# Kernel tuning notes

Hardware: AMD Instinct MI355X
Metric: run time of the kernel (lower is better)

The kernel has to match this reference:

```python
import jax, jax.numpy as jnp
import numpy as np

B, D, E, K = 16384, 1024, 8, 2  # tokens, embed_size, experts, top-k
W_IMPORTANCE = 0.01


def setup_inputs() -> dict:
    key = jax.random.key(0)
    ks = jax.random.split(key, 8)
    s = 1.0 / np.sqrt(D)
    return {
        "x": jax.random.normal(ks[0], (B, D), dtype=jnp.float32),   # fused vision features
        "q": jax.random.normal(ks[1], (B, D), dtype=jnp.float32),   # text features
        # cross-attention (seq_len=1) collapses to V then output projection
        "Wv": jax.random.normal(ks[2], (D, D), dtype=jnp.float32) * s,
        "bv": jnp.zeros((D,), dtype=jnp.float32),
        "Wo": jax.random.normal(ks[3], (D, D), dtype=jnp.float32) * s,
        "bo": jnp.zeros((D,), dtype=jnp.float32),
        # gate linear
        "Wg": jax.random.normal(ks[4], (D, E), dtype=jnp.float32) * s,
        "bg": jnp.zeros((E,), dtype=jnp.float32),
        # experts: Linear -> SiLU -> Linear
        "W1": jax.random.normal(ks[5], (E, D, D), dtype=jnp.float32) * s,
        "b1": jnp.zeros((E, D), dtype=jnp.float32),
        "W2": jax.random.normal(ks[6], (E, D, D), dtype=jnp.float32) * s,
        "b2": jnp.zeros((E, D), dtype=jnp.float32),
    }


def reference(x, q, Wv, bv, Wo, bo, Wg, bg, W1, b1, W2, b2):
    # CrossAttention with q_len = kv_len = 1: softmax over a single key is 1,
    # so attention output = out_proj(V(q)).
    att = (q @ Wv + bv) @ Wo + bo                      # (B, D)
    gate_logits = att @ Wg + bg                        # (B, E)
    gate_prob = jax.nn.softmax(gate_logits, axis=-1)   # eval mode: no noise
    top_w, top_i = jax.lax.top_k(gate_prob, K)         # (B, K)
    top_w = jax.nn.softmax(top_w, axis=-1)             # renormalize over top-k

    y = jnp.zeros_like(x)
    for e in range(E):  # small fixed expert count
        w_e = jnp.sum(jnp.where(top_i == e, top_w, 0.0), axis=-1)  # (B,)
        h = jax.nn.silu(x @ W1[e] + b1[e]) @ W2[e] + b2[e]         # (B, D)
        y = y + w_e[:, None] * h

    importance = gate_prob.sum(axis=0)  # (E,)
    importance_loss = W_IMPORTANCE * (jnp.std(importance, ddof=1) / jnp.mean(importance)) ** 2
    return y, gate_prob, importance_loss
```

## Files before the change

### kernel.cpp

```cpp
#include <hip/hip_runtime.h>
#include <hip/hip_bf16.h>

#define Btok 16384
#define Ddim 1024
#define Eexp 8

typedef __attribute__((ext_vector_type(8))) short short8;
typedef __attribute__((ext_vector_type(4))) float f32x4;

__device__ inline unsigned short f2bf(float f) {
    unsigned int u = __float_as_uint(f);
    unsigned int r = (u + 0x7fffu + ((u >> 16) & 1u)) >> 16;
    return (unsigned short)r;
}

__device__ inline void gload16(const void* g, void* l) {
    __builtin_amdgcn_global_load_lds(
        (const __attribute__((address_space(1))) void*)g,
        (__attribute__((address_space(3))) void*)l, 16, 0, 0);
}

#define MEMF() asm volatile("" ::: "memory")
#define BARRIER() do { MEMF(); __builtin_amdgcn_s_barrier(); MEMF(); } while (0)
#define VMW(n) do { asm volatile("s_waitcnt vmcnt(" #n ")" ::: "memory"); \
                    __builtin_amdgcn_sched_barrier(0); } while (0)

__global__ __launch_bounds__(256) void k_tmp(const float* __restrict__ Wo,
                                             const float* __restrict__ Wg,
                                             float* __restrict__ tmp) {
    int id = blockIdx.x * 256 + threadIdx.x;
    int d = id >> 3, e = id & 7;
    double s = 0.0;
    for (int k = 0; k < Ddim; ++k)
        s += (double)Wo[(long)d * Ddim + k] * (double)Wg[k * Eexp + e];
    tmp[id] = (float)s;
}

__global__ __launch_bounds__(256) void k_wc(const float* __restrict__ Wv,
                                            const float* __restrict__ tmp,
                                            float* __restrict__ WcT) {
    int id = blockIdx.x * 256 + threadIdx.x;
    int d = id >> 3, e = id & 7;
    double s = 0.0;
    for (int k = 0; k < Ddim; ++k)
        s += (double)Wv[(long)d * Ddim + k] * (double)tmp[k * Eexp + e];
    WcT[e * Ddim + d] = (float)s;
}

__global__ __launch_bounds__(512) void k_bc(const float* __restrict__ bv,
                                            const float* __restrict__ bo,
                                            const float* __restrict__ bg,
                                            const float* __restrict__ Wg,
                                            const float* __restrict__ tmp,
                                            float* __restrict__ bcomb) {
    int w = threadIdx.x >> 6, l = threadIdx.x & 63;
    double s = 0.0;
    for (int k = l; k < Ddim; k += 64)
        s += (double)bv[k] * (double)tmp[k * Eexp + w] +
             (double)bo[k] * (double)Wg[k * Eexp + w];
    #pragma unroll
    for (int off = 32; off; off >>= 1) s += __shfl_xor(s, off);
    if (l == 0) bcomb[w] = (float)s + bg[w];
}

__global__ __launch_bounds__(256) void k_convx(const float4* __restrict__ x,
                                               ushort4* __restrict__ xb) {
    int i = blockIdx.x * 256 + threadIdx.x;
    float4 v = x[i];
    ushort4 o;
    o.x = f2bf(v.x); o.y = f2bf(v.y); o.z = f2bf(v.z); o.w = f2bf(v.w);
    xb[i] = o;
}

__global__ __launch_bounds__(256) void k_convw(const float* __restrict__ W1,
                                               const float* __restrict__ W2,
                                               unsigned short* __restrict__ w1bT,
                                               unsigned short* __restrict__ w2bT) {
    __shared__ float tile[32][33];
    int bid = blockIdx.x;
    int arr = bid >> 13;
    int e = (bid >> 10) & 7, bi = (bid >> 5) & 31, bj = bid & 31;
    const float* src = (arr ? W2 : W1) + (long)e * Ddim * Ddim;
    unsigned short* dst = (arr ? w2bT : w1bT) + (long)e * Ddim * Ddim;
    int tr = threadIdx.x >> 5, tc = threadIdx.x & 31;
    #pragma unroll
    for (int i = 0; i < 4; ++i) {
        int dl = tr + i * 8;
        tile[dl][tc] = src[(long)(bi * 32 + dl) * Ddim + bj * 32 + tc];
    }
    __syncthreads();
    #pragma unroll
    for (int i = 0; i < 4; ++i) {
        int nl = tr + i * 8;
        dst[(long)(bj * 32 + nl) * Ddim + bi * 32 + tc] = f2bf(tile[tc][nl]);
    }
}

__global__ __launch_bounds__(256) void k_gate(const float* __restrict__ q,
                                              const float* __restrict__ WcT,
                                              const float* __restrict__ bcomb,
                                              float* __restrict__ gate_prob,
                                              int* __restrict__ choice,
                                              float2* __restrict__ w12,
                                              float* __restrict__ impP) {
    __shared__ float impL[4][8];
    int w = threadIdx.x >> 6, l = threadIdx.x & 63;
    int t = blockIdx.x * 4 + w;
    const float* qr = q + (long)t * Ddim;
    float acc[8] = {0, 0, 0, 0, 0, 0, 0, 0};
    #pragma unroll
    for (int i = 0; i < 4; ++i) {
        float4 qv = *(const float4*)(qr + (i * 64 + l) * 4);
        #pragma unroll
        for (int e = 0; e < 8; ++e) {
            float4 wv = *(const float4*)(WcT + e * Ddim + (i * 64 + l) * 4);
            acc[e] += qv.x * wv.x + qv.y * wv.y + qv.z * wv.z + qv.w * wv.w;
        }
    }
    #pragma unroll
    for (int off = 32; off; off >>= 1)
        #pragma unroll
        for (int e = 0; e < 8; ++e) acc[e] += __shfl_xor(acc[e], off);
    float lg[8], p[8];
    float m = -1e30f;
    #pragma unroll
    for (int e = 0; e < 8; ++e) { lg[e] = acc[e] + bcomb[e]; m = fmaxf(m, lg[e]); }
    float s = 0.f;
    #pragma unroll
    for (int e = 0; e < 8; ++e) { p[e] = expf(lg[e] - m); s += p[e]; }
    float inv = 1.f / s;
    #pragma unroll
    for (int e = 0; e < 8; ++e) p[e] *= inv;
    float p1 = -1.f, p2 = -1.f; int i1 = 0, i2 = 0;
    #pragma unroll
    for (int e = 0; e < 8; ++e) {
        float pe = p[e];
        if (pe > p1) { p2 = p1; i2 = i1; p1 = pe; i1 = e; }
        else if (pe > p2) { p2 = pe; i2 = e; }
    }
    float ee = expf(p2 - p1);
    float wa = 1.f / (1.f + ee);
    float wb = ee / (1.f + ee);
    if (l == 0) {
        #pragma unroll
        for (int e = 0; e < 8; ++e) gate_prob[(long)t * 8 + e] = p[e];
        #pragma unroll
        for (int e = 0; e < 8; ++e) impL[w][e] = p[e];
        choice[t] = i1 | (i2 << 8);
        w12[t] = make_float2(wa, wb);
    }
    __syncthreads();
    if (threadIdx.x < 8)
        impP[blockIdx.x * 8 + threadIdx.x] =
            impL[0][threadIdx.x] + impL[1][threadIdx.x] +
            impL[2][threadIdx.x] + impL[3][threadIdx.x];
}

__global__ __launch_bounds__(256) void k_hist(const int* __restrict__ choice,
                                              int* __restrict__ bcnt) {
    __shared__ int cnt[8];
    if (threadIdx.x < 8) cnt[threadIdx.x] = 0;
    __syncthreads();
    int ch = choice[blockIdx.x * 256 + threadIdx.x];
    atomicAdd(&cnt[ch & 255], 1);
    atomicAdd(&cnt[(ch >> 8) & 255], 1);
    __syncthreads();
    if (threadIdx.x < 8) bcnt[blockIdx.x * 8 + threadIdx.x] = cnt[threadIdx.x];
}

__global__ __launch_bounds__(512) void k_scan(const int* __restrict__ bcnt,
                                              int* __restrict__ bbase,
                                              int* __restrict__ counts) {
    int w = threadIdx.x >> 6, l = threadIdx.x & 63;
    int v = bcnt[l * 8 + w];
    int s = v;
    #pragma unroll
    for (int off = 1; off < 64; off <<= 1) {
        int o = __shfl_up(s, off);
        if (l >= off) s += o;
    }
    bbase[l * 8 + w] = s - v;
    if (l == 63) counts[w] = s;
}

__global__ __launch_bounds__(256) void k_scatter(const int* __restrict__ choice,
                                                 const float2* __restrict__ w12,
                                                 const int* __restrict__ bbase,
                                                 int* __restrict__ tok,
                                                 float* __restrict__ wgt) {
    __shared__ int wsum[4];
    int w = threadIdx.x >> 6, l = threadIdx.x & 63;
    int t = blockIdx.x * 256 + threadIdx.x;
    int ch = choice[t];
    int i1 = ch & 255, i2 = (ch >> 8) & 255;
    float2 ww = w12[t];
    for (int e = 0; e < 8; ++e) {
        bool f1 = (i1 == e), f2 = (i2 == e);
        bool f = f1 || f2;
        unsigned long long m = __ballot(f);
        int wl = __popcll(m & ((1ull << l) - 1ull));
        if (l == 0) wsum[w] = (int)__popcll(m);
        __syncthreads();
        int before = 0;
        #pragma unroll
        for (int j = 0; j < 4; ++j) before += (j < w) ? wsum[j] : 0;
        if (f) {
            int p = bbase[blockIdx.x * 8 + e] + before + wl;
            tok[e * Btok + p] = t;
            wgt[e * Btok + p] = f1 ? ww.x : ww.y;
        }
        __syncthreads();
    }
}

template <int MODE>
__global__ __launch_bounds__(256, 4) void k_gemm(const unsigned short* __restrict__ Abase,
                                                 const unsigned short* __restrict__ WT,
                                                 const float* __restrict__ bias,
                                                 const int* __restrict__ counts,
                                                 const int* __restrict__ tok,
                                                 const float* __restrict__ wgt,
                                                 unsigned short* __restrict__ Hout,
                                                 float* __restrict__ y) {
    __shared__ __align__(16) char lds[32768];
    char* ldsp = (char*)lds;

    int bid = blockIdx.x;
    int e = bid & 7;
    int k = bid >> 3;
    int rt = k >> 3, ct = k & 7;

    int n_e = counts[e];
    int r0 = rt * 128;
    if (r0 >= n_e) return;
    int off_e = 0;
    #pragma unroll
    for (int j = 0; j < 8; ++j) off_e += (j < e) ? counts[j] : 0;
    int n0 = ct * 128;

    int t = threadIdx.x;
    int w = t >> 6, l = t & 63;
    int wm = w >> 1, wn = w & 1;
    int t16 = t * 16;

    const char* sA[2]; const char* sB[2];
    {
        int q = (t & 7) ^ ((t >> 3) & 7);
        int h = q >> 2, c = q & 3;
        #pragma unroll
        for (int r = 0; r < 2; ++r) {
            int rowl = (t >> 3) + 32 * r + 64 * h;
            int idx = r0 + rowl; if (idx > n_e - 1) idx = n_e - 1;
            long g = (MODE == 0) ? (long)tok[e * Btok + idx] : (long)(off_e + idx);
            sA[r] = (const char*)Abase + g * 2048 + c * 16;
            sB[r] = (const char*)WT + ((long)e << 21) + (long)(n0 + rowl) * 2048 + c * 16;
        }
    }

    int rowb = (l & 15) * 128;
    int cpA = (((wm << 2) | (l >> 4)) ^ (l & 7)) << 4;
    int cpB = (((wn << 2) | (l >> 4)) ^ (l & 7)) << 4;

    f32x4 acc[4][4];
    #pragma unroll
    for (int mi = 0; mi < 4; ++mi)
        #pragma unroll
        for (int ni = 0; ni < 4; ++ni) acc[mi][ni] = {0.f, 0.f, 0.f, 0.f};

    auto stage = [&](int b) {
        gload16(sA[0], ldsp + b * 8192 + t16);
        gload16(sA[1], ldsp + b * 8192 + 4096 + t16);
        gload16(sB[0], ldsp + 16384 + b * 8192 + t16);
        gload16(sB[1], ldsp + 16384 + b * 8192 + 4096 + t16);
        sA[0] += 64; sA[1] += 64; sB[0] += 64; sB[1] += 64;
    };
    auto compute = [&](int b) {
        const char* pA = ldsp + b * 8192 + rowb;
        const char* pB = ldsp + 16384 + b * 8192 + rowb;
        short8 av[4], bv[4];
        #pragma unroll
        for (int mi = 0; mi < 4; ++mi) av[mi] = *(const short8*)(pA + mi * 2048 + cpA);
        #pragma unroll
        for (int ni = 0; ni < 4; ++ni) bv[ni] = *(const short8*)(pB + ni * 2048 + cpB);
        __builtin_amdgcn_s_setprio(1);
        #pragma unroll
        for (int mi = 0; mi < 4; ++mi)
            #pragma unroll
            for (int ni = 0; ni < 4; ++ni)
                acc[mi][ni] = __builtin_amdgcn_mfma_f32_16x16x32_bf16(av[mi], bv[ni], acc[mi][ni], 0, 0, 0);
        __builtin_amdgcn_s_setprio(0);
    };

    stage(0);
    stage(1);
    for (int kk = 0; kk < 31; ++kk) {
        VMW(4);
        BARRIER();
        compute(kk & 1);
        BARRIER();
        if (kk < 30) stage(kk & 1);
    }
    VMW(0); BARRIER();
    compute(1);

    float bias4[4];
    #pragma unroll
    for (int ni = 0; ni < 4; ++ni)
        bias4[ni] = bias[e * Ddim + n0 + wn * 64 + ni * 16 + (l & 15)];

    #pragma unroll
    for (int mi = 0; mi < 4; ++mi) {
        #pragma unroll
        for (int j = 0; j < 4; ++j) {
            int rl = wm * 64 + mi * 16 + (l >> 4) * 4 + j;
            int r = r0 + rl;
            bool ok = r < n_e;
            int trow = 0; float wr = 0.f;
            if (MODE == 1) {
                int ri = ok ? r : 0;
                trow = tok[e * Btok + ri];
                wr = wgt[e * Btok + ri];
            }
            #pragma unroll
            for (int ni = 0; ni < 4; ++ni) {
                int col = n0 + wn * 64 + ni * 16 + (l & 15);
                float v = acc[mi][ni][j] + bias4[ni];
                if (MODE == 0) {
                    v = v / (1.f + __expf(-v));
                    if (ok) Hout[(long)(off_e + r) * Ddim + col] = f2bf(v);
                } else {
                    if (ok) atomicAdd(&y[(long)trow * Ddim + col], wr * v);
                }
            }
        }
    }
}

__global__ __launch_bounds__(256) void k_loss(const float* __restrict__ impP,
                                              float* __restrict__ out) {
    __shared__ float red[256];
    __shared__ float impF[8];
    for (int e = 0; e < 8; ++e) {
        float s = 0.f;
        for (int i = threadIdx.x; i < 4096; i += 256) s += impP[i * 8 + e];
        red[threadIdx.x] = s;
        __syncthreads();
        for (int st = 128; st > 0; st >>= 1) {
            if ((int)threadIdx.x < st) red[threadIdx.x] += red[threadIdx.x + st];
            __syncthreads();
        }
        if (threadIdx.x == 0) impF[e] = red[0];
        __syncthreads();
    }
    if (threadIdx.x == 0) {
        double mean = 0.0;
        for (int e = 0; e < 8; ++e) mean += (double)impF[e];
        mean /= 8.0;
        double var = 0.0;
        for (int e = 0; e < 8; ++e) {
            double d = (double)impF[e] - mean;
            var += d * d;
        }
        var /= 7.0;
        out[0] = (float)(0.01 * var / (mean * mean));
    }
}

extern "C" void kernel_launch(void* const* d_in, const int* in_sizes, int n_in,
                              void* d_out, int out_size, void* d_ws, size_t ws_size,
                              hipStream_t stream) {
    const float* x  = (const float*)d_in[0];
    const float* q  = (const float*)d_in[1];
    const float* Wv = (const float*)d_in[2];
    const float* bv = (const float*)d_in[3];
    const float* Wo = (const float*)d_in[4];
    const float* bo = (const float*)d_in[5];
    const float* Wg = (const float*)d_in[6];
    const float* bg = (const float*)d_in[7];
    const float* W1 = (const float*)d_in[8];
    const float* b1 = (const float*)d_in[9];
    const float* W2 = (const float*)d_in[10];
    const float* b2 = (const float*)d_in[11];

    float* y = (float*)d_out;
    float* gate_prob = y + (long)Btok * Ddim;
    float* loss = gate_prob + (long)Btok * Eexp;

    char* ws = (char*)d_ws;
    int*   counts = (int*)(ws + 0);
    float* bcomb  = (float*)(ws + 256);
    float* tmp    = (float*)(ws + 512);
    float* WcT    = (float*)(ws + 33280);
    float* impP   = (float*)(ws + 66048);
    int*   choice = (int*)(ws + 197120);
    float2* w12   = (float2*)(ws + 262656);
    int*   tok    = (int*)(ws + 393728);
    float* wgt    = (float*)(ws + 918016);
    int*   bcnt   = (int*)(ws + 1442304);
    int*   bbase  = (int*)(ws + 1444352);
    unsigned short* xb   = (unsigned short*)(ws + 1446912);
    unsigned short* w1bT = (unsigned short*)(ws + 35001344);
    unsigned short* w2bT = (unsigned short*)(ws + 51778560);
    unsigned short* H    = (unsigned short*)(ws + 68555776);

    hipMemsetAsync(y, 0, (size_t)Btok * Ddim * sizeof(float), stream);

    k_tmp<<<32, 256, 0, stream>>>(Wo, Wg, tmp);
    k_wc <<<32, 256, 0, stream>>>(Wv, tmp, WcT);
    k_bc <<<1, 512, 0, stream>>>(bv, bo, bg, Wg, tmp, bcomb);
    k_convx<<<16384, 256, 0, stream>>>((const float4*)x, (ushort4*)xb);
    k_convw<<<16384, 256, 0, stream>>>(W1, W2, w1bT, w2bT);
    k_gate<<<4096, 256, 0, stream>>>(q, WcT, bcomb, gate_prob, choice, w12, impP);
    k_hist<<<64, 256, 0, stream>>>(choice, bcnt);
    k_scan<<<1, 512, 0, stream>>>(bcnt, bbase, counts);
    k_scatter<<<64, 256, 0, stream>>>(choice, w12, bbase, tok, wgt);
    k_gemm<0><<<4096, 256, 0, stream>>>(xb, w1bT, b1, counts, tok, wgt, H, nullptr);
    k_gemm<1><<<4096, 256, 0, stream>>>(H, w2bT, b2, counts, tok, wgt, nullptr, y);
    k_loss<<<1, 256, 0, stream>>>(impP, loss);
}
```

Baseline: 456.1 us.

## Enlarge expert GEMM tiles to 256x256 with 1024-thread blocks; merge conversion kernels

The expert GEMMs now use 256x256 output tiles computed by 16 waves per 1024-thread block, with 64KB of double-buffered LDS. Each wave still computes a 64x64 sub-tile, but each staged A/B tile is now reused by more waves, which cuts global traffic per FLOP. The x and weight bf16 conversions are merged into one launch. The cost is fewer blocks and lower occupancy per CU, plus more padding waste on the last, partially filled row tile of each expert.

```diff
diff --git a/kernel.cpp b/kernel.cpp
--- a/kernel.cpp
+++ b/kernel.cpp
@@ -63,21 +63,22 @@
     if (l == 0) bcomb[w] = (float)s + bg[w];
 }
 
-__global__ __launch_bounds__(256) void k_convx(const float4* __restrict__ x,
-                                               ushort4* __restrict__ xb) {
-    int i = blockIdx.x * 256 + threadIdx.x;
-    float4 v = x[i];
-    ushort4 o;
-    o.x = f2bf(v.x); o.y = f2bf(v.y); o.z = f2bf(v.z); o.w = f2bf(v.w);
-    xb[i] = o;
-}
-
-__global__ __launch_bounds__(256) void k_convw(const float* __restrict__ W1,
-                                               const float* __restrict__ W2,
-                                               unsigned short* __restrict__ w1bT,
-                                               unsigned short* __restrict__ w2bT) {
+__global__ __launch_bounds__(256) void k_conv(const float* __restrict__ W1,
+                                              const float* __restrict__ W2,
+                                              unsigned short* __restrict__ w1bT,
+                                              unsigned short* __restrict__ w2bT,
+                                              const float4* __restrict__ x,
+                                              ushort4* __restrict__ xb) {
     __shared__ float tile[32][33];
     int bid = blockIdx.x;
+    if (bid >= 16384) {
+        int i = (bid - 16384) * 256 + threadIdx.x;
+        float4 v = x[i];
+        ushort4 o;
+        o.x = f2bf(v.x); o.y = f2bf(v.y); o.z = f2bf(v.z); o.w = f2bf(v.w);
+        xb[i] = o;
+        return;
+    }
     int arr = bid >> 13;
     int e = (bid >> 10) & 7, bi = (bid >> 5) & 31, bj = bid & 31;
     const float* src = (arr ? W2 : W1) + (long)e * Ddim * Ddim;
@@ -214,52 +215,51 @@
 }
 
 template <int MODE>
-__global__ __launch_bounds__(256, 4) void k_gemm(const unsigned short* __restrict__ Abase,
-                                                 const unsigned short* __restrict__ WT,
-                                                 const float* __restrict__ bias,
-                                                 const int* __restrict__ counts,
-                                                 const int* __restrict__ tok,
-                                                 const float* __restrict__ wgt,
-                                                 unsigned short* __restrict__ Hout,
-                                                 float* __restrict__ y) {
-    __shared__ __align__(16) char lds[32768];
+__global__ __launch_bounds__(1024, 4) void k_gemm(const unsigned short* __restrict__ Abase,
+                                                  const unsigned short* __restrict__ WT,
+                                                  const float* __restrict__ bias,
+                                                  const int* __restrict__ counts,
+                                                  const int* __restrict__ tok,
+                                                  const float* __restrict__ wgt,
+                                                  unsigned short* __restrict__ Hout,
+                                                  float* __restrict__ y) {
+    __shared__ __align__(16) char lds[65536];
     char* ldsp = (char*)lds;
 
     int bid = blockIdx.x;
     int e = bid & 7;
-    int k = bid >> 3;
-    int rt = k >> 3, ct = k & 7;
+    int kb = bid >> 3;
+    int rt = kb >> 2, ct = kb & 3;
 
     int n_e = counts[e];
-    int r0 = rt * 128;
+    int r0 = rt * 256;
     if (r0 >= n_e) return;
     int off_e = 0;
     #pragma unroll
     for (int j = 0; j < 8; ++j) off_e += (j < e) ? counts[j] : 0;
-    int n0 = ct * 128;
+    int n0 = ct * 256;
 
     int t = threadIdx.x;
     int w = t >> 6, l = t & 63;
-    int wm = w >> 1, wn = w & 1;
+    int wm = w >> 2, wn = w & 3;
+
+    const char* sA; const char* sB;
+    {
+        int line = t >> 3, p = t & 7;
+        int qq = p ^ (line & 7);
+        int rowl = line + 128 * (qq >> 2);
+        int c = qq & 3;
+        int idx = r0 + rowl; if (idx > n_e - 1) idx = n_e - 1;
+        long g = (MODE == 0) ? (long)tok[e * Btok + idx] : (long)(off_e + idx);
+        sA = (const char*)Abase + g * 2048 + c * 16;
+        sB = (const char*)WT + ((long)e << 21) + (long)(n0 + rowl) * 2048 + c * 16;
+    }
     int t16 = t * 16;
 
-    const char* sA[2]; const char* sB[2];
-    {
-        int q = (t & 7) ^ ((t >> 3) & 7);
-        int h = q >> 2, c = q & 3;
-        #pragma unroll
-        for (int r = 0; r < 2; ++r) {
-            int rowl = (t >> 3) + 32 * r + 64 * h;
-            int idx = r0 + rowl; if (idx > n_e - 1) idx = n_e - 1;
-            long g = (MODE == 0) ? (long)tok[e * Btok + idx] : (long)(off_e + idx);
-            sA[r] = (const char*)Abase + g * 2048 + c * 16;
-            sB[r] = (const char*)WT + ((long)e << 21) + (long)(n0 + rowl) * 2048 + c * 16;
-        }
-    }
-
-    int rowb = (l & 15) * 128;
-    int cpA = (((wm << 2) | (l >> 4)) ^ (l & 7)) << 4;
-    int cpB = (((wn << 2) | (l >> 4)) ^ (l & 7)) << 4;
+    int laA = ((wm & 1) * 64 + (l & 15)) * 128;
+    int slA = ((((wm >> 1) << 2) | (l >> 4)) ^ (l & 7)) << 4;
+    int laB = ((wn & 1) * 64 + (l & 15)) * 128;
+    int slB = ((((wn >> 1) << 2) | (l >> 4)) ^ (l & 7)) << 4;
 
     f32x4 acc[4][4];
     #pragma unroll
@@ -267,21 +267,19 @@
         #pragma unroll
         for (int ni = 0; ni < 4; ++ni) acc[mi][ni] = {0.f, 0.f, 0.f, 0.f};
 
-    auto stage = [&](int b) {
-        gload16(sA[0], ldsp + b * 8192 + t16);
-        gload16(sA[1], ldsp + b * 8192 + 4096 + t16);
-        gload16(sB[0], ldsp + 16384 + b * 8192 + t16);
-        gload16(sB[1], ldsp + 16384 + b * 8192 + 4096 + t16);
-        sA[0] += 64; sA[1] += 64; sB[0] += 64; sB[1] += 64;
+    auto stage = [&](int bb) {
+        gload16(sA, ldsp + bb + t16);
+        gload16(sB, ldsp + bb + 16384 + t16);
+        sA += 64; sB += 64;
     };
-    auto compute = [&](int b) {
-        const char* pA = ldsp + b * 8192 + rowb;
-        const char* pB = ldsp + 16384 + b * 8192 + rowb;
+    auto compute = [&](int bb) {
         short8 av[4], bv[4];
         #pragma unroll
-        for (int mi = 0; mi < 4; ++mi) av[mi] = *(const short8*)(pA + mi * 2048 + cpA);
-        #pragma unroll
-        for (int ni = 0; ni < 4; ++ni) bv[ni] = *(const short8*)(pB + ni * 2048 + cpB);
+        for (int mi = 0; mi < 4; ++mi)
+            av[mi] = *(const short8*)(ldsp + bb + laA + mi * 2048 + slA);
+        #pragma unroll
+        for (int ni = 0; ni < 4; ++ni)
+            bv[ni] = *(const short8*)(ldsp + bb + 16384 + laB + ni * 2048 + slB);
         __builtin_amdgcn_s_setprio(1);
         #pragma unroll
         for (int mi = 0; mi < 4; ++mi)
@@ -292,16 +290,18 @@
     };
 
     stage(0);
-    stage(1);
+    stage(32768);
+    #pragma unroll 1
     for (int kk = 0; kk < 31; ++kk) {
-        VMW(4);
+        VMW(2);
         BARRIER();
-        compute(kk & 1);
+        int bb = (kk & 1) * 32768;
+        compute(bb);
         BARRIER();
-        if (kk < 30) stage(kk & 1);
+        if (kk < 30) stage(bb);
     }
     VMW(0); BARRIER();
-    compute(1);
+    compute(32768);
 
     float bias4[4];
     #pragma unroll
@@ -408,13 +408,12 @@
     k_tmp<<<32, 256, 0, stream>>>(Wo, Wg, tmp);
     k_wc <<<32, 256, 0, stream>>>(Wv, tmp, WcT);
     k_bc <<<1, 512, 0, stream>>>(bv, bo, bg, Wg, tmp, bcomb);
-    k_convx<<<16384, 256, 0, stream>>>((const float4*)x, (ushort4*)xb);
-    k_convw<<<16384, 256, 0, stream>>>(W1, W2, w1bT, w2bT);
+    k_conv<<<32768, 256, 0, stream>>>(W1, W2, w1bT, w2bT, (const float4*)x, (ushort4*)xb);
     k_gate<<<4096, 256, 0, stream>>>(q, WcT, bcomb, gate_prob, choice, w12, impP);
     k_hist<<<64, 256, 0, stream>>>(choice, bcnt);
     k_scan<<<1, 512, 0, stream>>>(bcnt, bbase, counts);
     k_scatter<<<64, 256, 0, stream>>>(choice, w12, bbase, tok, wgt);
-    k_gemm<0><<<4096, 256, 0, stream>>>(xb, w1bT, b1, counts, tok, wgt, H, nullptr);
-    k_gemm<1><<<4096, 256, 0, stream>>>(H, w2bT, b2, counts, tok, wgt, nullptr, y);
+    k_gemm<0><<<1024, 1024, 0, stream>>>(xb, w1bT, b1, counts, tok, wgt, H, nullptr);
+    k_gemm<1><<<1024, 1024, 0, stream>>>(H, w2bT, b2, counts, tok, wgt, nullptr, y);
     k_loss<<<1, 256, 0, stream>>>(impP, loss);
 }
```

Measured after the change: 513.1 us. +12.5%, slower.
